# Kernel optimization log

Measured on AMD Instinct MI355X. Metric: run time of the kernel, lower is better.

Reference implementation:

```python
import jax, jax.numpy as jnp
import numpy as np

N_NODES = 50000  # nodes in the (sub)graph


def setup_inputs() -> dict:
    key = jax.random.key(0)
    ks = jax.random.split(key, 8)
    nodes = jax.random.randint(ks[0], (N_NODES,), 0, 100000)
    src = jax.random.randint(ks[1], (800000,), 0, N_NODES)
    dst = jax.random.randint(ks[2], (800000,), 0, N_NODES)
    emb = jax.random.normal(ks[3], (100000, 256), dtype=jnp.float32)
    W = jax.random.normal(ks[4], (256, 128), dtype=jnp.float32) * 0.05
    b = jax.random.normal(ks[5], (128,), dtype=jnp.float32) * 0.05
    mlp_w = jax.random.normal(ks[6], (128, 40), dtype=jnp.float32) * 0.05
    mlp_b = jax.random.normal(ks[7], (40,), dtype=jnp.float32) * 0.05
    return {"nodes": nodes, "src": src, "dst": dst, "emb": emb,
            "W": W, "b": b, "mlp_w": mlp_w, "mlp_b": mlp_b}


def reference(nodes, src, dst, emb, W, b, mlp_w, mlp_b):
    n = N_NODES
    ones = jnp.ones_like(src, dtype=jnp.float32)
    out_deg = jax.ops.segment_sum(ones, src, num_segments=n)  # src out-degree
    in_deg = jax.ops.segment_sum(ones, dst, num_segments=n)   # dst in-degree
    norm_src = jax.lax.rsqrt(jnp.maximum(out_deg, 1.0))       # D_out^{-1/2}
    norm_dst = jax.lax.rsqrt(jnp.maximum(in_deg, 1.0))        # D_in^{-1/2}

    feat = emb[nodes]                                          # [N, in_dim]
    # dgl GraphConv(norm='both'): in_dim > out_dim -> project first, then aggregate
    h = (feat * norm_src[:, None]) @ W                         # [N, out_dim]
    agg = jax.ops.segment_sum(h[src], dst, num_segments=n)     # SpMM: sum over in-edges
    feat_out = agg * norm_dst[:, None] + b                     # [N, out_dim]

    logits = feat_out @ mlp_w + mlp_b                          # [N, num_classes]
    return (feat_out, logits)
```

## Files before the change

kernel.cpp:

```cpp
#include <hip/hip_runtime.h>

#define IN_DIM 256
#define OUT_DIM 128
#define N_CLS 40

#define SLICE 8192
#define NE_CH 20

typedef __attribute__((ext_vector_type(8))) short short8;
typedef __attribute__((ext_vector_type(4))) float floatx4;

static __device__ __forceinline__ unsigned short f2bf(float f) {
    union { float f; unsigned u; } v; v.f = f;
    unsigned r = v.u + 0x7FFF + ((v.u >> 16) & 1);
    return (unsigned short)(r >> 16);
}

__global__ __launch_bounds__(256) void hist_wconv_kernel(
    const int* __restrict__ src, const int* __restrict__ dst,
    int* __restrict__ partial_out, int* __restrict__ partial_in,
    const float* __restrict__ W, unsigned short* __restrict__ Wt,
    int ne, int n, int chunk, int nbh)
{
    __shared__ __align__(16) int lh_out[SLICE];
    __shared__ __align__(16) int lh_in[SLICE];

    const int tid = threadIdx.x;

    if (blockIdx.x >= nbh) {
        int t = (blockIdx.x - nbh) * 256 + tid;
        if (t < IN_DIM * OUT_DIM) {
            int k = t >> 7, c = t & 127;
            Wt[c * IN_DIM + k] = f2bf(W[t]);
        }
        return;
    }

    const int s = blockIdx.x / NE_CH;
    const int e = blockIdx.x % NE_CH;
    const int lo = s * SLICE;
    const int hi = min(lo + SLICE, n);

    for (int i = tid; i < SLICE; i += 256) { lh_out[i] = 0; lh_in[i] = 0; }
    __syncthreads();

    const int start = e * chunk;
    const int end = min(start + chunk, ne);
    const int cnt4 = (end - start) >> 2;
    const int4* s4 = (const int4*)(src + start);
    const int4* d4 = (const int4*)(dst + start);
    for (int k = tid; k < cnt4; k += 256) {
        int4 sv = s4[k];
        int4 dv = d4[k];
        unsigned q;
        q = (unsigned)(sv.x - lo); if (q < SLICE) atomicAdd(&lh_out[q], 1);
        q = (unsigned)(sv.y - lo); if (q < SLICE) atomicAdd(&lh_out[q], 1);
        q = (unsigned)(sv.z - lo); if (q < SLICE) atomicAdd(&lh_out[q], 1);
        q = (unsigned)(sv.w - lo); if (q < SLICE) atomicAdd(&lh_out[q], 1);
        q = (unsigned)(dv.x - lo); if (q < SLICE) atomicAdd(&lh_in[q], 1);
        q = (unsigned)(dv.y - lo); if (q < SLICE) atomicAdd(&lh_in[q], 1);
        q = (unsigned)(dv.z - lo); if (q < SLICE) atomicAdd(&lh_in[q], 1);
        q = (unsigned)(dv.w - lo); if (q < SLICE) atomicAdd(&lh_in[q], 1);
    }
    for (int t = start + (cnt4 << 2) + tid; t < end; t += 256) {
        unsigned q;
        q = (unsigned)(src[t] - lo); if (q < SLICE) atomicAdd(&lh_out[q], 1);
        q = (unsigned)(dst[t] - lo); if (q < SLICE) atomicAdd(&lh_in[q], 1);
    }
    __syncthreads();

    const int cnt = hi - lo;
    const int c4 = cnt >> 2;
    int4* po = (int4*)(partial_out + (size_t)e * n + lo);
    int4* pi = (int4*)(partial_in + (size_t)e * n + lo);
    for (int i = tid; i < c4; i += 256) {
        po[i] = ((const int4*)lh_out)[i];
        pi[i] = ((const int4*)lh_in)[i];
    }
    for (int i = (c4 << 2) + tid; i < cnt; i += 256) {
        partial_out[(size_t)e * n + lo + i] = lh_out[i];
        partial_in[(size_t)e * n + lo + i] = lh_in[i];
    }
}

__global__ __launch_bounds__(256) void reduce_kernel(
    int* __restrict__ partial_out, int* __restrict__ partial_in,
    int* __restrict__ cnt_out, int* __restrict__ cnt_in, int n)
{
    const int g = blockIdx.x * 256 + threadIdx.x;
    const int ng4 = n >> 2;
    if (g < ng4) {
        const size_t base = (size_t)g * 4;
        int4 sum = make_int4(0, 0, 0, 0);
#pragma unroll
        for (int e = 0; e < NE_CH; e++) {
            int4 v = *(const int4*)(partial_out + (size_t)e * n + base);
            sum.x += v.x; sum.y += v.y; sum.z += v.z; sum.w += v.w;
        }
        *(int4*)(cnt_out + base) = sum;

        int4 run = make_int4(0, 0, 0, 0);
#pragma unroll
        for (int e = 0; e < NE_CH; e++) {
            int* p = partial_in + (size_t)e * n + base;
            int4 v = *(const int4*)p;
            *(int4*)p = run;
            run.x += v.x; run.y += v.y; run.z += v.z; run.w += v.w;
        }
        *(int4*)(cnt_in + base) = run;
    }
    const int t = (ng4 << 2) + g;
    if (t < n) {
        int sum = 0;
#pragma unroll
        for (int e = 0; e < NE_CH; e++) sum += partial_out[(size_t)e * n + t];
        cnt_out[t] = sum;
        int run = 0;
#pragma unroll
        for (int e = 0; e < NE_CH; e++) {
            int v = partial_in[(size_t)e * n + t];
            partial_in[(size_t)e * n + t] = run;
            run += v;
        }
        cnt_in[t] = run;
    }
}

__global__ __launch_bounds__(1024) void scan_kernel(
    const int* __restrict__ cnt, int* __restrict__ row_start, int n)
{
    __shared__ int wsum[16];
    __shared__ int carry_s;
    const int tid = threadIdx.x;
    const int lane = tid & 63, wid = tid >> 6;
    if (tid == 0) carry_s = 0;
    __syncthreads();

    for (int chunk = 0; chunk < n; chunk += 8192) {
        int base = chunk + tid * 8;
        int v[8];
        if (base + 8 <= n) {
            int4 a = *(const int4*)&cnt[base];
            int4 b = *(const int4*)&cnt[base + 4];
            v[0]=a.x; v[1]=a.y; v[2]=a.z; v[3]=a.w;
            v[4]=b.x; v[5]=b.y; v[6]=b.z; v[7]=b.w;
        } else {
#pragma unroll
            for (int t = 0; t < 8; t++) v[t] = (base + t < n) ? cnt[base + t] : 0;
        }
        int tsum = 0;
#pragma unroll
        for (int t = 0; t < 8; t++) tsum += v[t];

        int incl = tsum;
#pragma unroll
        for (int off = 1; off < 64; off <<= 1) {
            int q = __shfl_up(incl, (unsigned)off, 64);
            if (lane >= off) incl += q;
        }
        if (lane == 63) wsum[wid] = incl;
        __syncthreads();
        int woff = 0;
        for (int w = 0; w < wid; ++w) woff += wsum[w];
        int carry = carry_s;
        int run = carry + woff + (incl - tsum);
        if (base + 8 <= n) {
            int o[8];
#pragma unroll
            for (int t = 0; t < 8; t++) { o[t] = run; run += v[t]; }
            int4 r0, r1;
            r0.x=o[0]; r0.y=o[1]; r0.z=o[2]; r0.w=o[3];
            r1.x=o[4]; r1.y=o[5]; r1.z=o[6]; r1.w=o[7];
            *(int4*)&row_start[base]     = r0;
            *(int4*)&row_start[base + 4] = r1;
        } else {
#pragma unroll
            for (int t = 0; t < 8; t++) {
                if (base + t < n) row_start[base + t] = run;
                run += v[t];
            }
        }
        __syncthreads();
        if (tid == 1023) carry_s = carry + woff + incl;
        __syncthreads();
    }
    if (tid == 0) row_start[n] = carry_s;
}

__global__ __launch_bounds__(256) void scatter_lds_kernel(
    const int* __restrict__ src, const int* __restrict__ dst,
    const int* __restrict__ row_start, const int* __restrict__ prefix_in,
    int* __restrict__ csr_src, int ne, int n, int chunk)
{
    __shared__ __align__(16) int cur[SLICE];

    const int tid = threadIdx.x;
    const int s = blockIdx.x / NE_CH;
    const int e = blockIdx.x % NE_CH;
    const int lo = s * SLICE;
    const int hi = min(lo + SLICE, n);
    const int cnt = hi - lo;

    const int c4 = cnt >> 2;
    for (int i = tid; i < c4; i += 256) {
        int4 rs = *(const int4*)(row_start + lo + i * 4);
        int4 pf = *(const int4*)(prefix_in + (size_t)e * n + lo + i * 4);
        rs.x += pf.x; rs.y += pf.y; rs.z += pf.z; rs.w += pf.w;
        ((int4*)cur)[i] = rs;
    }
    for (int i = (c4 << 2) + tid; i < cnt; i += 256)
        cur[i] = row_start[lo + i] + prefix_in[(size_t)e * n + lo + i];
    __syncthreads();

    const int start = e * chunk;
    const int end = min(start + chunk, ne);
    const int cnt4e = (end - start) >> 2;
    const int4* s4 = (const int4*)(src + start);
    const int4* d4 = (const int4*)(dst + start);
    for (int k = tid; k < cnt4e; k += 256) {
        int4 sv = s4[k];
        int4 dv = d4[k];
        unsigned q;
        q = (unsigned)(dv.x - lo); if (q < SLICE) csr_src[atomicAdd(&cur[q], 1)] = sv.x;
        q = (unsigned)(dv.y - lo); if (q < SLICE) csr_src[atomicAdd(&cur[q], 1)] = sv.y;
        q = (unsigned)(dv.z - lo); if (q < SLICE) csr_src[atomicAdd(&cur[q], 1)] = sv.z;
        q = (unsigned)(dv.w - lo); if (q < SLICE) csr_src[atomicAdd(&cur[q], 1)] = sv.w;
    }
    for (int t = start + (cnt4e << 2) + tid; t < end; t += 256) {
        unsigned q = (unsigned)(dst[t] - lo);
        if (q < SLICE) csr_src[atomicAdd(&cur[q], 1)] = src[t];
    }
}

__global__ __launch_bounds__(256) void gemm1_mfma_kernel(
    const int* __restrict__ nodes, const float* __restrict__ emb,
    const unsigned short* __restrict__ Wt, const int* __restrict__ cnt_out,
    unsigned short* __restrict__ h, int n)
{
    __shared__ unsigned short A_lds[64 * 40];
    __shared__ unsigned short B_lds[128 * 40];
    __shared__ int   snode[64];
    __shared__ float sscale[64];

    const int tid = threadIdx.x;
    const int m0  = blockIdx.x * 64;

    if (tid < 64) {
        int gr = m0 + tid;
        snode[tid]  = (gr < n) ? nodes[gr] : 0;
        sscale[tid] = (gr < n) ? rsqrtf(fmaxf((float)cnt_out[gr], 1.0f)) : 0.0f;
    }
    __syncthreads();

    const int arow = tid >> 2, aq = tid & 3;
    const int bcol = tid >> 1, bh = tid & 1;
    const float* aptr = emb + (size_t)snode[arow] * IN_DIM + aq * 8;
    const unsigned short* bptr = Wt + bcol * IN_DIM + bh * 16;

    float    ar[8];
    unsigned bw[8];

#define LOAD_REGS(KK) do {                                          \
        const floatx4 v0 = *(const floatx4*)(aptr + (KK) * 32);     \
        const floatx4 v1 = *(const floatx4*)(aptr + (KK) * 32 + 4); \
        ar[0]=v0[0]; ar[1]=v0[1]; ar[2]=v0[2]; ar[3]=v0[3];         \
        ar[4]=v1[0]; ar[5]=v1[1]; ar[6]=v1[2]; ar[7]=v1[3];         \
        const uint4 w0 = *(const uint4*)(bptr + (KK) * 32);         \
        const uint4 w1 = *(const uint4*)(bptr + (KK) * 32 + 8);     \
        bw[0]=w0.x; bw[1]=w0.y; bw[2]=w0.z; bw[3]=w0.w;             \
        bw[4]=w1.x; bw[5]=w1.y; bw[6]=w1.z; bw[7]=w1.w;             \
    } while (0)

#define WRITE_LDS() do {                                            \
        union { unsigned short s[8]; uint4 v; } ua;                 \
        _Pragma("unroll")                                           \
        for (int i = 0; i < 8; i++) ua.s[i] = f2bf(ar[i]);          \
        *(uint4*)&A_lds[arow * 40 + aq * 8] = ua.v;                 \
        uint4 b0, b1;                                               \
        b0.x=bw[0]; b0.y=bw[1]; b0.z=bw[2]; b0.w=bw[3];             \
        b1.x=bw[4]; b1.y=bw[5]; b1.z=bw[6]; b1.w=bw[7];             \
        *(uint4*)&B_lds[bcol * 40 + bh * 16]     = b0;              \
        *(uint4*)&B_lds[bcol * 40 + bh * 16 + 8] = b1;              \
    } while (0)

    const int wave = tid >> 6, lane = tid & 63;
    const int rbase = (wave & 1) * 32 + (lane & 15);
    const int cbase = (wave >> 1) * 64 + (lane & 15);
    const int koff  = (lane >> 4) * 8;

    floatx4 acc[2][4];
#pragma unroll
    for (int i = 0; i < 2; i++)
#pragma unroll
        for (int j = 0; j < 4; j++) acc[i][j] = (floatx4){0.f, 0.f, 0.f, 0.f};

    LOAD_REGS(0);
    WRITE_LDS();

    for (int kk = 0; kk < 8; ++kk) {
        if (kk < 7) LOAD_REGS(kk + 1);
        __syncthreads();
        short8 af0 = *(const short8*)&A_lds[rbase * 40 + koff];
        short8 af1 = *(const short8*)&A_lds[(rbase + 16) * 40 + koff];
        short8 bf[4];
#pragma unroll
        for (int ct = 0; ct < 4; ct++)
            bf[ct] = *(const short8*)&B_lds[(cbase + ct * 16) * 40 + koff];
#pragma unroll
        for (int ct = 0; ct < 4; ct++) {
            acc[0][ct] = __builtin_amdgcn_mfma_f32_16x16x32_bf16(bf[ct], af0, acc[0][ct], 0, 0, 0);
            acc[1][ct] = __builtin_amdgcn_mfma_f32_16x16x32_bf16(bf[ct], af1, acc[1][ct], 0, 0, 0);
        }
        __syncthreads();
        if (kk < 7) WRITE_LDS();
    }

#pragma unroll
    for (int rt = 0; rt < 2; rt++) {
        int lrow = (wave & 1) * 32 + rt * 16 + (lane & 15);
        int grow = m0 + lrow;
        float sc = sscale[lrow];
        if (grow < n) {
#pragma unroll
            for (int ct = 0; ct < 4; ct++) {
                int col = (wave >> 1) * 64 + ct * 16 + (lane >> 4) * 4;
                union { unsigned short s[4]; uint2 v; } o;
                o.s[0] = f2bf(acc[rt][ct][0] * sc);
                o.s[1] = f2bf(acc[rt][ct][1] * sc);
                o.s[2] = f2bf(acc[rt][ct][2] * sc);
                o.s[3] = f2bf(acc[rt][ct][3] * sc);
                *(uint2*)&h[(size_t)grow * OUT_DIM + col] = o.v;
            }
        }
    }
#undef LOAD_REGS
#undef WRITE_LDS
}

__global__ __launch_bounds__(256) void spmm_csr_kernel(
    const int* __restrict__ row_start, const int* __restrict__ csr_src,
    const unsigned short* __restrict__ h, const float* __restrict__ bias,
    float* __restrict__ out_feat, int n)
{
    const int lane = threadIdx.x & 63;
    const int c2 = lane * 2;
    const int row = blockIdx.x * 4 + (threadIdx.x >> 6);
    if (row >= n) return;

    const int rs = row_start[row];
    const int re = row_start[row + 1];
    const int deg = re - rs;

    float aL[4] = {0.f, 0.f, 0.f, 0.f};
    float aH[4] = {0.f, 0.f, 0.f, 0.f};

    for (int base = 0; base < deg; base += 64) {
        const int cnt = min(deg - base, 64);
        int idx = (lane < cnt) ? csr_src[rs + base + lane] : 0;
        int t = 0;
        for (; t + 7 < cnt; t += 8) {
            int s[8];
#pragma unroll
            for (int u = 0; u < 8; u++) s[u] = __shfl(idx, t + u, 64);
            unsigned v[8];
#pragma unroll
            for (int u = 0; u < 8; u++)
                v[u] = *(const unsigned*)&h[(size_t)s[u] * OUT_DIM + c2];
#pragma unroll
            for (int u = 0; u < 8; u++) {
                union { unsigned uu; float f; } x, y;
                x.uu = v[u] << 16;
                y.uu = v[u] & 0xffff0000u;
                aL[u & 3] += x.f;
                aH[u & 3] += y.f;
            }
        }
        for (; t + 3 < cnt; t += 4) {
            int s[4];
#pragma unroll
            for (int u = 0; u < 4; u++) s[u] = __shfl(idx, t + u, 64);
            unsigned v[4];
#pragma unroll
            for (int u = 0; u < 4; u++)
                v[u] = *(const unsigned*)&h[(size_t)s[u] * OUT_DIM + c2];
#pragma unroll
            for (int u = 0; u < 4; u++) {
                union { unsigned uu; float f; } x, y;
                x.uu = v[u] << 16;
                y.uu = v[u] & 0xffff0000u;
                aL[u] += x.f;
                aH[u] += y.f;
            }
        }
        for (; t < cnt; ++t) {
            int s0 = __shfl(idx, t, 64);
            unsigned v0 = *(const unsigned*)&h[(size_t)s0 * OUT_DIM + c2];
            union { unsigned uu; float f; } x, y;
            x.uu = v0 << 16;
            y.uu = v0 & 0xffff0000u;
            aL[0] += x.f;
            aH[0] += y.f;
        }
    }

    const float nd = rsqrtf(fmaxf((float)deg, 1.0f));
    const float f0 = ((aL[0] + aL[1]) + (aL[2] + aL[3])) * nd + bias[c2];
    const float f1 = ((aH[0] + aH[1]) + (aH[2] + aH[3])) * nd + bias[c2 + 1];
    *(float2*)&out_feat[(size_t)row * OUT_DIM + c2] = make_float2(f0, f1);
}

__global__ __launch_bounds__(256) void mlp_mfma_kernel(
    const float* __restrict__ F, const float* __restrict__ mlp_w,
    const float* __restrict__ mlp_b, float* __restrict__ out_logits, int n)
{
    __shared__ unsigned short A_lds[48 * 136];
    __shared__ float s_mlpb[48];

    const int tid = threadIdx.x;
    for (int i = tid; i < 48 * 128; i += 256) {
        int cls = i >> 7, k = i & 127;
        A_lds[cls * 136 + k] =
            (cls < N_CLS) ? f2bf(mlp_w[(size_t)k * N_CLS + cls]) : (unsigned short)0;
    }
    if (tid < 48) s_mlpb[tid] = (tid < N_CLS) ? mlp_b[tid] : 0.f;
    __syncthreads();

    const int wave = tid >> 6, lane = tid & 63;
    const int r = lane & 15, koff = (lane >> 4) * 8;
    const int row = blockIdx.x * 64 + wave * 16 + r;
    const int rowc = (row < n) ? row : (n - 1);
    const float* fp = F + (size_t)rowc * OUT_DIM + koff;

    floatx4 acc[3];
#pragma unroll
    for (int ct = 0; ct < 3; ct++) acc[ct] = (floatx4){0.f, 0.f, 0.f, 0.f};

#pragma unroll
    for (int kk = 0; kk < 4; kk++) {
        floatx4 v0 = *(const floatx4*)(fp + kk * 32);
        floatx4 v1 = *(const floatx4*)(fp + kk * 32 + 4);
        union { unsigned short s[8]; short8 v; } bfr;
#pragma unroll
        for (int i = 0; i < 4; i++) {
            bfr.s[i]     = f2bf(v0[i]);
            bfr.s[4 + i] = f2bf(v1[i]);
        }
#pragma unroll
        for (int ct = 0; ct < 3; ct++) {
            short8 af = *(const short8*)&A_lds[(ct * 16 + r) * 136 + kk * 32 + koff];
            acc[ct] = __builtin_amdgcn_mfma_f32_16x16x32_bf16(af, bfr.v, acc[ct], 0, 0, 0);
        }
    }

    if (row < n) {
#pragma unroll
        for (int ct = 0; ct < 3; ct++)
#pragma unroll
            for (int i = 0; i < 4; i++) {
                int cls = ct * 16 + (lane >> 4) * 4 + i;
                if (cls < N_CLS)
                    out_logits[(size_t)row * N_CLS + cls] = acc[ct][i] + s_mlpb[cls];
            }
    }
}

extern "C" void kernel_launch(void* const* d_in, const int* in_sizes, int n_in,
                              void* d_out, int out_size, void* d_ws, size_t ws_size,
                              hipStream_t stream) {
    const int*   nodes = (const int*)d_in[0];
    const int*   src   = (const int*)d_in[1];
    const int*   dst   = (const int*)d_in[2];
    const float* emb   = (const float*)d_in[3];
    const float* W     = (const float*)d_in[4];
    const float* b     = (const float*)d_in[5];
    const float* mlp_w = (const float*)d_in[6];
    const float* mlp_b = (const float*)d_in[7];

    const int n  = in_sizes[0];
    const int ne = in_sizes[1];

    int* cnt_out     = (int*)d_ws;
    int* cnt_in      = cnt_out + n;
    int* row_start   = cnt_in + n;
    int* csr_src     = row_start + n + 8;
    int* partial_out = csr_src + ne;
    int* partial_in  = partial_out + (size_t)NE_CH * n;
    size_t off = ((size_t)(3 * n + 8) + (size_t)ne + 2 * (size_t)NE_CH * n) * sizeof(int);
    off = (off + 15) & ~(size_t)15;
    unsigned short* Wt = (unsigned short*)((char*)d_ws + off);
    off += (size_t)IN_DIM * OUT_DIM * sizeof(unsigned short);
    off = (off + 15) & ~(size_t)15;
    unsigned short* h = (unsigned short*)((char*)d_ws + off);

    float* out_feat   = (float*)d_out;
    float* out_logits = out_feat + (size_t)n * OUT_DIM;

    const int ns = (n + SLICE - 1) / SLICE;
    const int chunk = (((ne + NE_CH - 1) / NE_CH) + 3) & ~3;
    const int nbh = ns * NE_CH;
    const int nbw = (IN_DIM * OUT_DIM + 255) / 256;

    hist_wconv_kernel<<<nbh + nbw, 256, 0, stream>>>(
        src, dst, partial_out, partial_in, W, Wt, ne, n, chunk, nbh);
    reduce_kernel<<<((n >> 2) + 255) / 256, 256, 0, stream>>>(
        partial_out, partial_in, cnt_out, cnt_in, n);
    scan_kernel<<<1, 1024, 0, stream>>>(cnt_in, row_start, n);
    scatter_lds_kernel<<<nbh, 256, 0, stream>>>(
        src, dst, row_start, partial_in, csr_src, ne, n, chunk);
    gemm1_mfma_kernel<<<(n + 63) / 64, 256, 0, stream>>>(nodes, emb, Wt, cnt_out, h, n);
    spmm_csr_kernel<<<(n + 3) / 4, 256, 0, stream>>>(
        row_start, csr_src, h, b, out_feat, n);
    mlp_mfma_kernel<<<(n + 63) / 64, 256, 0, stream>>>(
        out_feat, mlp_w, mlp_b, out_logits, n);
}
```

Before: 150.4 us.

## Enlarge GEMM tile to 128 rows, unroll SpMM gather deeper, use nontemporal stores

The projection GEMM now processes 128 rows per block with a 4x4 MFMA tile per wave. The W tile is loaded once per 128 rows instead of once per 64, which halves redundant B loads and raises MFMA work per LDS read. The SpMM inner gather is unrolled to 16 loads in flight to increase memory-level parallelism. Output stores in SpMM and the MLP use nontemporal hints to avoid polluting cache. The larger tile raises register pressure and halves the GEMM grid size, which may reduce occupancy.

```diff
diff --git a/kernel.cpp b/kernel.cpp
--- a/kernel.cpp
+++ b/kernel.cpp
@@ -237,60 +237,62 @@
     const unsigned short* __restrict__ Wt, const int* __restrict__ cnt_out,
     unsigned short* __restrict__ h, int n)
 {
-    __shared__ unsigned short A_lds[64 * 40];
+    __shared__ unsigned short A_lds[128 * 40];
     __shared__ unsigned short B_lds[128 * 40];
-    __shared__ int   snode[64];
-    __shared__ float sscale[64];
+    __shared__ int   snode[128];
+    __shared__ float sscale[128];
 
     const int tid = threadIdx.x;
-    const int m0  = blockIdx.x * 64;
-
-    if (tid < 64) {
+    const int m0  = blockIdx.x * 128;
+
+    if (tid < 128) {
         int gr = m0 + tid;
         snode[tid]  = (gr < n) ? nodes[gr] : 0;
         sscale[tid] = (gr < n) ? rsqrtf(fmaxf((float)cnt_out[gr], 1.0f)) : 0.0f;
     }
     __syncthreads();
 
-    const int arow = tid >> 2, aq = tid & 3;
-    const int bcol = tid >> 1, bh = tid & 1;
-    const float* aptr = emb + (size_t)snode[arow] * IN_DIM + aq * 8;
-    const unsigned short* bptr = Wt + bcol * IN_DIM + bh * 16;
-
-    float    ar[8];
+    const int arow = tid >> 1, aq = tid & 1;
+    const float* aptr = emb + (size_t)snode[arow] * IN_DIM + aq * 16;
+    const unsigned short* bptr = Wt + arow * IN_DIM + aq * 16;
+
+    float    ar[16];
     unsigned bw[8];
 
-#define LOAD_REGS(KK) do {                                          \
-        const floatx4 v0 = *(const floatx4*)(aptr + (KK) * 32);     \
-        const floatx4 v1 = *(const floatx4*)(aptr + (KK) * 32 + 4); \
-        ar[0]=v0[0]; ar[1]=v0[1]; ar[2]=v0[2]; ar[3]=v0[3];         \
-        ar[4]=v1[0]; ar[5]=v1[1]; ar[6]=v1[2]; ar[7]=v1[3];         \
-        const uint4 w0 = *(const uint4*)(bptr + (KK) * 32);         \
-        const uint4 w1 = *(const uint4*)(bptr + (KK) * 32 + 8);     \
-        bw[0]=w0.x; bw[1]=w0.y; bw[2]=w0.z; bw[3]=w0.w;             \
-        bw[4]=w1.x; bw[5]=w1.y; bw[6]=w1.z; bw[7]=w1.w;             \
+#define LOAD_REGS(KK) do {                                           \
+        _Pragma("unroll")                                            \
+        for (int q = 0; q < 4; q++) {                                \
+            const floatx4 v = *(const floatx4*)(aptr + (KK) * 32 + q * 4); \
+            ar[q*4+0]=v[0]; ar[q*4+1]=v[1]; ar[q*4+2]=v[2]; ar[q*4+3]=v[3]; \
+        }                                                            \
+        const uint4 w0 = *(const uint4*)(bptr + (KK) * 32);          \
+        const uint4 w1 = *(const uint4*)(bptr + (KK) * 32 + 8);      \
+        bw[0]=w0.x; bw[1]=w0.y; bw[2]=w0.z; bw[3]=w0.w;              \
+        bw[4]=w1.x; bw[5]=w1.y; bw[6]=w1.z; bw[7]=w1.w;              \
     } while (0)
 
-#define WRITE_LDS() do {                                            \
-        union { unsigned short s[8]; uint4 v; } ua;                 \
-        _Pragma("unroll")                                           \
-        for (int i = 0; i < 8; i++) ua.s[i] = f2bf(ar[i]);          \
-        *(uint4*)&A_lds[arow * 40 + aq * 8] = ua.v;                 \
-        uint4 b0, b1;                                               \
-        b0.x=bw[0]; b0.y=bw[1]; b0.z=bw[2]; b0.w=bw[3];             \
-        b1.x=bw[4]; b1.y=bw[5]; b1.z=bw[6]; b1.w=bw[7];             \
-        *(uint4*)&B_lds[bcol * 40 + bh * 16]     = b0;              \
-        *(uint4*)&B_lds[bcol * 40 + bh * 16 + 8] = b1;              \
+#define WRITE_LDS() do {                                             \
+        union { unsigned short s[16]; uint4 v[2]; } ua;              \
+        _Pragma("unroll")                                            \
+        for (int i = 0; i < 16; i++) ua.s[i] = f2bf(ar[i]);          \
+        *(uint4*)&A_lds[arow * 40 + aq * 16]     = ua.v[0];          \
+        *(uint4*)&A_lds[arow * 40 + aq * 16 + 8] = ua.v[1];          \
+        uint4 b0, b1;                                                \
+        b0.x=bw[0]; b0.y=bw[1]; b0.z=bw[2]; b0.w=bw[3];              \
+        b1.x=bw[4]; b1.y=bw[5]; b1.z=bw[6]; b1.w=bw[7];              \
+        *(uint4*)&B_lds[arow * 40 + aq * 16]     = b0;               \
+        *(uint4*)&B_lds[arow * 40 + aq * 16 + 8] = b1;               \
     } while (0)
 
     const int wave = tid >> 6, lane = tid & 63;
-    const int rbase = (wave & 1) * 32 + (lane & 15);
-    const int cbase = (wave >> 1) * 64 + (lane & 15);
-    const int koff  = (lane >> 4) * 8;
-
-    floatx4 acc[2][4];
-#pragma unroll
-    for (int i = 0; i < 2; i++)
+    const int wr = (wave & 1) * 64;
+    const int wc = (wave >> 1) * 64;
+    const int fr = lane & 15;
+    const int koff = (lane >> 4) * 8;
+
+    floatx4 acc[4][4];
+#pragma unroll
+    for (int i = 0; i < 4; i++)
 #pragma unroll
         for (int j = 0; j < 4; j++) acc[i][j] = (floatx4){0.f, 0.f, 0.f, 0.f};
 
@@ -300,30 +302,31 @@
     for (int kk = 0; kk < 8; ++kk) {
         if (kk < 7) LOAD_REGS(kk + 1);
         __syncthreads();
-        short8 af0 = *(const short8*)&A_lds[rbase * 40 + koff];
-        short8 af1 = *(const short8*)&A_lds[(rbase + 16) * 40 + koff];
-        short8 bf[4];
-#pragma unroll
-        for (int ct = 0; ct < 4; ct++)
-            bf[ct] = *(const short8*)&B_lds[(cbase + ct * 16) * 40 + koff];
-#pragma unroll
-        for (int ct = 0; ct < 4; ct++) {
-            acc[0][ct] = __builtin_amdgcn_mfma_f32_16x16x32_bf16(bf[ct], af0, acc[0][ct], 0, 0, 0);
-            acc[1][ct] = __builtin_amdgcn_mfma_f32_16x16x32_bf16(bf[ct], af1, acc[1][ct], 0, 0, 0);
-        }
+        short8 af[4], bf[4];
+#pragma unroll
+        for (int t = 0; t < 4; t++) {
+            af[t] = *(const short8*)&A_lds[(wr + t * 16 + fr) * 40 + koff];
+            bf[t] = *(const short8*)&B_lds[(wc + t * 16 + fr) * 40 + koff];
+        }
+#pragma unroll
+        for (int rt = 0; rt < 4; rt++)
+#pragma unroll
+            for (int ct = 0; ct < 4; ct++)
+                acc[rt][ct] = __builtin_amdgcn_mfma_f32_16x16x32_bf16(
+                    bf[ct], af[rt], acc[rt][ct], 0, 0, 0);
         __syncthreads();
         if (kk < 7) WRITE_LDS();
     }
 
 #pragma unroll
-    for (int rt = 0; rt < 2; rt++) {
-        int lrow = (wave & 1) * 32 + rt * 16 + (lane & 15);
+    for (int rt = 0; rt < 4; rt++) {
+        int lrow = wr + rt * 16 + fr;
         int grow = m0 + lrow;
         float sc = sscale[lrow];
         if (grow < n) {
 #pragma unroll
             for (int ct = 0; ct < 4; ct++) {
-                int col = (wave >> 1) * 64 + ct * 16 + (lane >> 4) * 4;
+                int col = wc + ct * 16 + (lane >> 4) * 4;
                 union { unsigned short s[4]; uint2 v; } o;
                 o.s[0] = f2bf(acc[rt][ct][0] * sc);
                 o.s[1] = f2bf(acc[rt][ct][1] * sc);
@@ -358,16 +361,16 @@
         const int cnt = min(deg - base, 64);
         int idx = (lane < cnt) ? csr_src[rs + base + lane] : 0;
         int t = 0;
-        for (; t + 7 < cnt; t += 8) {
-            int s[8];
-#pragma unroll
-            for (int u = 0; u < 8; u++) s[u] = __shfl(idx, t + u, 64);
-            unsigned v[8];
-#pragma unroll
-            for (int u = 0; u < 8; u++)
+        for (; t + 15 < cnt; t += 16) {
+            int s[16];
+#pragma unroll
+            for (int u = 0; u < 16; u++) s[u] = __shfl(idx, t + u, 64);
+            unsigned v[16];
+#pragma unroll
+            for (int u = 0; u < 16; u++)
                 v[u] = *(const unsigned*)&h[(size_t)s[u] * OUT_DIM + c2];
 #pragma unroll
-            for (int u = 0; u < 8; u++) {
+            for (int u = 0; u < 16; u++) {
                 union { unsigned uu; float f; } x, y;
                 x.uu = v[u] << 16;
                 y.uu = v[u] & 0xffff0000u;
@@ -406,7 +409,10 @@
     const float nd = rsqrtf(fmaxf((float)deg, 1.0f));
     const float f0 = ((aL[0] + aL[1]) + (aL[2] + aL[3])) * nd + bias[c2];
     const float f1 = ((aH[0] + aH[1]) + (aH[2] + aH[3])) * nd + bias[c2 + 1];
-    *(float2*)&out_feat[(size_t)row * OUT_DIM + c2] = make_float2(f0, f1);
+    union { float f[2]; unsigned long long u; } o;
+    o.f[0] = f0; o.f[1] = f1;
+    __builtin_nontemporal_store(o.u,
+        (unsigned long long*)&out_feat[(size_t)row * OUT_DIM + c2]);
 }
 
 __global__ __launch_bounds__(256) void mlp_mfma_kernel(
@@ -459,7 +465,8 @@
             for (int i = 0; i < 4; i++) {
                 int cls = ct * 16 + (lane >> 4) * 4 + i;
                 if (cls < N_CLS)
-                    out_logits[(size_t)row * N_CLS + cls] = acc[ct][i] + s_mlpb[cls];
+                    __builtin_nontemporal_store(acc[ct][i] + s_mlpb[cls],
+                        &out_logits[(size_t)row * N_CLS + cls]);
             }
     }
 }
@@ -507,7 +514,7 @@
     scan_kernel<<<1, 1024, 0, stream>>>(cnt_in, row_start, n);
     scatter_lds_kernel<<<nbh, 256, 0, stream>>>(
         src, dst, row_start, partial_in, csr_src, ne, n, chunk);
-    gemm1_mfma_kernel<<<(n + 63) / 64, 256, 0, stream>>>(nodes, emb, Wt, cnt_out, h, n);
+    gemm1_mfma_kernel<<<(n + 127) / 128, 256, 0, stream>>>(nodes, emb, Wt, cnt_out, h, n);
     spmm_csr_kernel<<<(n + 3) / 4, 256, 0, stream>>>(
         row_start, csr_src, h, b, out_feat, n);
     mlp_mfma_kernel<<<(n + 63) / 64, 256, 0, stream>>>(
```

Result: no change. 152.0 us (+1.1%).
